# Optimization experiments

Hardware: AMD Instinct MI355X
Metric: run time of the kernel (lower is better)

Reference implementation:

```python
import jax, jax.numpy as jnp
import numpy as np

N = 120000   # current nodes
F = 256      # num_feat
H = 256      # num_hidden
L = 64       # num_logits
E_MP = 1000000  # message-passing edges
E = 200000      # scored edges
PREV = [60000, 80000, 100000]
PROX_WEIGHT = 0.3


def setup_inputs() -> dict:
    key = jax.random.key(0)
    ks = jax.random.split(key, 40)
    n = lambda k, shape, s=0.05: jax.random.normal(k, shape, dtype=jnp.float32) * s
    inp = {}
    inp["x"] = n(ks[0], (N, F), 1.0)
    inp["mp_adj"] = jax.random.randint(ks[1], (2, E_MP), 0, N)
    inp["edges"] = jax.random.randint(ks[2], (2, E), 0, N)
    inp["index"] = jax.random.randint(ks[3], (E,), 0, E)
    inp["prev_emb0"] = n(ks[4], (PREV[0], H), 1.0)
    inp["prev_emb1"] = n(ks[5], (PREV[1], H), 1.0)
    inp["prev_emb2"] = n(ks[6], (PREV[2], H), 1.0)
    # Module_L params
    inp["gc1_W"] = n(ks[7], (F, H))
    inp["gc1_b"] = jnp.zeros((H,), jnp.float32)
    inp["gc2_W"] = n(ks[8], (H, H))
    inp["gc2_b"] = jnp.zeros((H,), jnp.float32)
    inp["linear_W"] = n(ks[9], (2 * H, H))
    inp["linear_b"] = jnp.zeros((H,), jnp.float32)
    inp["weight_lin"] = n(ks[10], (H, H))
    inp["bias_lin"] = jnp.zeros((H,), jnp.float32)
    inp["w_q"] = n(ks[11], (H, H))
    inp["w_k"] = n(ks[12], (H, H))
    inp["w_v"] = n(ks[13], (H, H))
    # ensemble params
    inp["ml_w1"] = n(ks[14], (2 * H, H)); inp["ml_b1"] = jnp.zeros((H,), jnp.float32)
    inp["ml_w2"] = n(ks[15], (H, 1));     inp["ml_b2"] = jnp.zeros((1,), jnp.float32)
    inp["ms_w1"] = n(ks[16], (2 * H, H)); inp["ms_b1"] = jnp.zeros((H,), jnp.float32)
    inp["ms_w2"] = n(ks[17], (H, 1));     inp["ms_b2"] = jnp.zeros((1,), jnp.float32)
    inp["msdr_w"] = n(ks[18], (L, H));    inp["msdr_b"] = jnp.zeros((H,), jnp.float32)
    # Module_S logits and precomputed score tables
    inp["logits"] = n(ks[19], (N, L), 1.0)
    inp["ms_train_score"] = jax.random.uniform(ks[20], (E,), dtype=jnp.float32)
    inp["prox_train_score"] = jax.random.uniform(ks[21], (E,), dtype=jnp.float32)
    return inp


def _gcn(x, W, b, src, dst, n_nodes):
    xw = x @ W
    loop = jnp.arange(n_nodes)
    s = jnp.concatenate([src, loop])
    d = jnp.concatenate([dst, loop])
    deg = jax.ops.segment_sum(jnp.ones_like(d, dtype=xw.dtype), d, num_segments=n_nodes)
    dinv = jax.lax.rsqrt(jnp.maximum(deg, 1.0))
    norm = (dinv[s] * dinv[d])[:, None]
    out = jax.ops.segment_sum(xw[s] * norm, d, num_segments=n_nodes)
    return out + b


def _mean_max(a, b):
    return jnp.concatenate([(a + b) * 0.5, jnp.maximum(a, b)], axis=1)


def reference(x, mp_adj, edges, index, prev_emb0, prev_emb1, prev_emb2,
              gc1_W, gc1_b, gc2_W, gc2_b, linear_W, linear_b,
              weight_lin, bias_lin, w_q, w_k, w_v,
              ml_w1, ml_b1, ml_w2, ml_b2, ms_w1, ms_b1, ms_w2, ms_b2,
              msdr_w, msdr_b, logits, ms_train_score, prox_train_score):
    src_mp, dst_mp = mp_adj[0], mp_adj[1]
    # --- Module_L: 2-layer GCN encoder (dropout = identity in eval) ---
    h = jnp.tanh(_gcn(x, gc1_W, gc1_b, src_mp, dst_mp, N))
    emb = jnp.tanh(_gcn(h, gc2_W, gc2_b, src_mp, dst_mp, N))

    # --- ragged per-window temporal attention over previous snapshots ---
    prev = [prev_emb0, prev_emb1, prev_emb2]
    T = len(prev)
    start = 0
    parts = []
    for i in range(T):
        end = prev[i].shape[0]
        if end == N:
            break
        # stack snapshots i..T-1 plus current, restricted to window [start:end)
        stack = jnp.stack([prev[j][start:end] for j in range(i, T)] + [emb[start:end]], axis=0)  # [S,n,H]
        q = emb[start:end] @ w_q              # [n,H]
        k = stack @ w_k                        # [S,n,H]
        v = stack @ w_v                        # [S,n,H]
        attn = jnp.einsum('nh,snh->ns', q, k) / np.sqrt(np.float32(H))
        w = jax.nn.softmax(attn, axis=-1)      # [n,S]
        parts.append(jnp.einsum('ns,snh->nh', w, v))
        start = end
    if start != N:
        parts.append(emb[start:] @ w_v)
    attn_emb = jnp.concatenate(parts, axis=0)  # [N,H]

    emb2 = jnp.tanh(jnp.concatenate([emb, attn_emb], axis=1) @ linear_W + linear_b)  # [N,H]

    # --- symmetric bilinear edge scores ---
    sym = (weight_lin + weight_lin.T) * 0.5
    es, ed = edges[0], edges[1]
    sim = ((emb2[es] @ sym) * emb2[ed] + bias_lin).sum(axis=1)
    ml_scores = jax.nn.sigmoid(sim)            # [E]

    # --- Module_S / Proximity: table lookups ---
    ms_scores = ms_train_score[index]
    prox_scores = prox_train_score[index]

    # --- ensemble weighted sum ---
    scores = jnp.stack([ml_scores, ms_scores, prox_scores], axis=1)  # [E,3]
    ml_feat = _mean_max(emb2[es], emb2[ed])                          # [E,2H]
    a_ml = jnp.tanh(jnp.tanh(ml_feat @ ml_w1 + ml_b1) @ ml_w2 + ml_b2)
    r0 = jnp.tanh(logits[es] @ msdr_w + msdr_b)
    r1 = jnp.tanh(logits[ed] @ msdr_w + msdr_b)
    a_ms = jnp.tanh(jnp.tanh(_mean_max(r0, r1) @ ms_w1 + ms_b1) @ ms_w2 + ms_b2)
    a_px = jnp.full_like(a_ml, PROX_WEIGHT)
    attn_w = jax.nn.softmax(jnp.concatenate([a_ml, a_ms, a_px], axis=1), axis=1)  # [E,3]
    final = jnp.clip((scores * attn_w).sum(axis=1), 0.0, 1.0)
    return final
```

## Files before the change

### kernel.cpp

```cpp
#include <hip/hip_runtime.h>
#include <hip/hip_bf16.h>

#define Nn_   120000
#define F_    256
#define H_    256
#define L_    64
#define EMP_  1000000
#define E_    200000
#define P0_   60000
#define P1_   80000
#define P2_   100000
#define PROXW 0.3f

typedef __attribute__((ext_vector_type(8))) short bf16x8;
typedef __attribute__((ext_vector_type(4))) float f32x4;

__device__ inline float bf2f(unsigned short u) {
    union { unsigned int i; float f; } x; x.i = ((unsigned int)u) << 16; return x.f;
}
__device__ inline unsigned short f2bf(float f) {
    union { float f; unsigned int i; } x; x.f = f;
    unsigned int r = x.i + 0x7fffu + ((x.i >> 16) & 1u);
    return (unsigned short)(r >> 16);
}
__device__ inline float tanh_fast(float x) {
    float e = __expf(2.0f * x);
    return 1.0f - 2.0f * __builtin_amdgcn_rcpf(e + 1.0f);
}
__device__ inline float sigmoid_fast(float z) {
    return __builtin_amdgcn_rcpf(1.0f + __expf(-z));
}
__device__ inline int lds_off(int row, int s) {
    return row * 64 + ((s ^ ((row >> 1) & 3)) << 4);
}
__device__ inline void gload_lds16(const void* g, void* l) {
    __builtin_amdgcn_global_load_lds((const __attribute__((address_space(1))) void*)g,
                                     (__attribute__((address_space(3))) void*)l, 16, 0, 0);
}
__device__ inline void unpk8(uint4 u, float* o) {
    o[0] = bf2f(u.x & 0xffff); o[1] = bf2f(u.x >> 16);
    o[2] = bf2f(u.y & 0xffff); o[3] = bf2f(u.y >> 16);
    o[4] = bf2f(u.z & 0xffff); o[5] = bf2f(u.z >> 16);
    o[6] = bf2f(u.w & 0xffff); o[7] = bf2f(u.w >> 16);
}
__device__ inline void meanmax_u(unsigned int ua, unsigned int ub,
                                 unsigned int& um, unsigned int& ux) {
    float alo = __uint_as_float(ua << 16);
    float ahi = __uint_as_float(ua & 0xffff0000u);
    float blo = __uint_as_float(ub << 16);
    float bhi = __uint_as_float(ub & 0xffff0000u);
    um = (unsigned int)f2bf((alo + blo) * 0.5f) |
         ((unsigned int)f2bf((ahi + bhi) * 0.5f) << 16);
    ux = (__float_as_uint(fmaxf(alo, blo)) >> 16) |
         (__float_as_uint(fmaxf(ahi, bhi)) & 0xffff0000u);
}
__device__ inline float dot2_u(unsigned int ug, unsigned int ub) {
    float gl = __uint_as_float(ug << 16);
    float gh = __uint_as_float(ug & 0xffff0000u);
    float bl = __uint_as_float(ub << 16);
    float bh = __uint_as_float(ub & 0xffff0000u);
    return fmaf(gl, bl, gh * bh);
}

__global__ void k_count(const int* __restrict__ dst, int* __restrict__ cnt, int n) {
    int e = blockIdx.x * 256 + threadIdx.x;
    if (e < n) atomicAdd(&cnt[dst[e]], 1);
}
__global__ void k_block_reduce(const int* __restrict__ cnt, int* __restrict__ bsum, int n) {
    __shared__ int s[256];
    int i = blockIdx.x * 256 + threadIdx.x;
    s[threadIdx.x] = (i < n) ? cnt[i] : 0;
    __syncthreads();
    for (int o = 128; o > 0; o >>= 1) {
        if (threadIdx.x < o) s[threadIdx.x] += s[threadIdx.x + o];
        __syncthreads();
    }
    if (threadIdx.x == 0) bsum[blockIdx.x] = s[0];
}
__global__ void k_scan_bsum(int* bsum, int nb) {
    if (threadIdx.x == 0 && blockIdx.x == 0) {
        int acc = 0;
        for (int i = 0; i < nb; i++) { int v = bsum[i]; bsum[i] = acc; acc += v; }
    }
}
__global__ void k_scan_final(const int* __restrict__ cnt, const int* __restrict__ bsum,
                             int* __restrict__ rowp, int n, int etot) {
    __shared__ int s[256];
    int tid = threadIdx.x;
    int i = blockIdx.x * 256 + tid;
    int v = (i < n) ? cnt[i] : 0;
    s[tid] = v;
    __syncthreads();
    for (int o = 1; o < 256; o <<= 1) {
        int t = 0;
        if (tid >= o) t = s[tid - o];
        __syncthreads();
        s[tid] += t;
        __syncthreads();
    }
    if (i < n) rowp[i] = bsum[blockIdx.x] + s[tid] - v;
    if (i == 0 && blockIdx.x == 0) rowp[n] = etot;
}
__global__ void k_fill(const int* __restrict__ src, const int* __restrict__ dst,
                       const int* __restrict__ rowp, int* __restrict__ fill,
                       int* __restrict__ csr, int n) {
    int e = blockIdx.x * 256 + threadIdx.x;
    if (e < n) {
        int d = dst[e];
        int p = atomicAdd(&fill[d], 1);
        csr[rowp[d] + p] = src[e];
    }
}
__global__ void k_dinv(const int* __restrict__ cnt, float* __restrict__ dinv, int n) {
    int i = blockIdx.x * 256 + threadIdx.x;
    if (i < n) dinv[i] = rsqrtf((float)cnt[i] + 1.0f);
}

#define TM 64
#define TN 64
#define TK 16
template <bool TRANSB>
__global__ void gemm_tiled(const float* __restrict__ A, const float* __restrict__ B,
                           float* __restrict__ C, int M, int K, int N) {
    __shared__ float As[TK][TM + 4];
    __shared__ float Bs[TK][TN + 4];
    int tid = threadIdx.x;
    int tx = tid & 15, ty = tid >> 4;
    int row0 = blockIdx.y * TM, col0 = blockIdx.x * TN;
    int lr = tid >> 2, lc4 = (tid & 3) * 4;
    float acc[4][4] = {};
    for (int k0 = 0; k0 < K; k0 += TK) {
        {
            int gr = row0 + lr;
            float4 v = make_float4(0.f, 0.f, 0.f, 0.f);
            if (gr < M) v = *(const float4*)(A + (size_t)gr * K + k0 + lc4);
            As[lc4 + 0][lr] = v.x; As[lc4 + 1][lr] = v.y;
            As[lc4 + 2][lr] = v.z; As[lc4 + 3][lr] = v.w;
        }
        {
            int n = tid & 63, kk0 = tid >> 6;
#pragma unroll
            for (int p = 0; p < 4; p++) {
                int kk = kk0 + p * 4;
                if (TRANSB) Bs[kk][n] = B[(size_t)(col0 + n) * K + k0 + kk];
                else        Bs[kk][n] = B[(size_t)(k0 + kk) * N + col0 + n];
            }
        }
        __syncthreads();
#pragma unroll
        for (int kk = 0; kk < TK; kk++) {
            float4 a = *(const float4*)&As[kk][ty * 4];
            float4 b = *(const float4*)&Bs[kk][tx * 4];
            float av[4] = {a.x, a.y, a.z, a.w};
            float bv[4] = {b.x, b.y, b.z, b.w};
#pragma unroll
            for (int i = 0; i < 4; i++)
#pragma unroll
                for (int j = 0; j < 4; j++) acc[i][j] += av[i] * bv[j];
        }
        __syncthreads();
    }
#pragma unroll
    for (int i = 0; i < 4; i++) {
        int r = row0 + ty * 4 + i;
        if (r >= M) continue;
#pragma unroll
        for (int j = 0; j < 4; j++) C[(size_t)r * N + col0 + tx * 4 + j] = acc[i][j];
    }
}

__global__ void k_cvt(const float* __restrict__ in, unsigned short* __restrict__ out, int n4) {
    int i = blockIdx.x * 256 + threadIdx.x;
    if (i >= n4) return;
    float4 v = ((const float4*)in)[i];
    ushort4 o;
    o.x = f2bf(v.x); o.y = f2bf(v.y); o.z = f2bf(v.z); o.w = f2bf(v.w);
    ((ushort4*)out)[i] = o;
}

__device__ inline void packBF_task(const float* __restrict__ Wsrc,
                                   unsigned short* __restrict__ P, int blk) {
    int t = blk * 256 + threadIdx.x;
    int c = t >> 6, l = t & 63;
    int os = c >> 5, half = (c >> 4) & 1, colb = c & 15;
    int col = (colb << 4) + (l & 15);
    int k = (half << 8) + (os << 5) + ((l >> 4) << 3);
    bf16x8 v;
#pragma unroll
    for (int j = 0; j < 8; ++j) v[j] = (short)f2bf(Wsrc[(size_t)(k + j) * 256 + col]);
    *(bf16x8*)(P + (size_t)t * 8) = v;
}

__global__ void k_prep1(const float* __restrict__ gc1W, const float* __restrict__ gc2W,
                        const float* __restrict__ msdrW, const float* __restrict__ wlin,
                        const float* __restrict__ blin, const float* __restrict__ mlw1,
                        const float* __restrict__ msw1,
                        unsigned short* __restrict__ gc1Wt, unsigned short* __restrict__ gc2Wt,
                        unsigned short* __restrict__ msdrWt, unsigned short* __restrict__ symb,
                        float* __restrict__ sumb, unsigned short* __restrict__ mlPk,
                        unsigned short* __restrict__ msPk) {
    __shared__ float s[256];
    int b = blockIdx.x, tid = threadIdx.x;
    if (b < 256) {
        int c = b;
        for (int r = tid; r < 256; r += 256) gc1Wt[c * 256 + r] = f2bf(gc1W[(size_t)r * 256 + c]);
    } else if (b < 512) {
        int c = b - 256;
        for (int r = tid; r < 256; r += 256) gc2Wt[c * 256 + r] = f2bf(gc2W[(size_t)r * 256 + c]);
    } else if (b < 768) {
        int c = b - 512;
        if (tid < 64) msdrWt[c * 64 + tid] = f2bf(msdrW[(size_t)tid * 256 + c]);
    } else if (b < 1024) {
        int r = b - 768, c = tid;
        symb[r * 256 + c] = f2bf(0.5f * (wlin[r * 256 + c] + wlin[c * 256 + r]));
    } else if (b == 1024) {
        s[tid] = blin[tid];
        __syncthreads();
        for (int o = 128; o > 0; o >>= 1) {
            if (tid < o) s[tid] += s[tid + o];
            __syncthreads();
        }
        if (tid == 0) sumb[0] = s[0];
    } else if (b < 1089) {
        packBF_task(mlw1, mlPk, b - 1025);
    } else {
        packBF_task(msw1, msPk, b - 1089);
    }
}
__global__ void k_prep2(const float* __restrict__ Mqk, const float* __restrict__ linW,
                        const float* __restrict__ W2w, unsigned short* __restrict__ MqkT,
                        unsigned short* __restrict__ Bt) {
    int b = blockIdx.x, tid = threadIdx.x;
    if (b < 256) {
        int c = b;
        for (int r = tid; r < 256; r += 256) MqkT[c * 256 + r] = f2bf(Mqk[(size_t)r * 256 + c]);
    } else {
        int idx = (b - 256) * 256 + tid;
        int n = idx >> 9, k = idx & 511;
        float v = (k < 256) ? linW[(size_t)k * 256 + n] : W2w[(size_t)(k - 256) * 256 + n];
        Bt[idx] = f2bf(v);
    }
}

__global__ __launch_bounds__(256)
void k_agg_bf(const unsigned short* __restrict__ xw, const int* __restrict__ rowp,
              const int* __restrict__ csr, const float* __restrict__ dinv,
              const float* __restrict__ bias, unsigned short* __restrict__ out) {
    int w = threadIdx.x >> 6, lane = threadIdx.x & 63;
    int v = blockIdx.x * 4 + w;
    if (v >= Nn_) return;
    const uint2* x64 = (const uint2*)xw;
    uint2 us = x64[(size_t)v * 64 + lane];
    float dv = dinv[v];
    float4 bv = *(const float4*)(bias + lane * 4);
    float a0 = 0.f, a1 = 0.f, a2 = 0.f, a3 = 0.f;
    int beg = rowp[v], end = rowp[v + 1];
    uint2 u0 = make_uint2(0, 0), u1 = make_uint2(0, 0);
    uint2 u2 = make_uint2(0, 0), u3 = make_uint2(0, 0);
    float e0 = 0.f, e1 = 0.f, e2 = 0.f, e3 = 0.f;
    if (beg < end)     { int s = csr[beg];     e0 = dinv[s]; u0 = x64[(size_t)s * 64 + lane]; }
    if (beg + 1 < end) { int s = csr[beg + 1]; e1 = dinv[s]; u1 = x64[(size_t)s * 64 + lane]; }
    if (beg + 2 < end) { int s = csr[beg + 2]; e2 = dinv[s]; u2 = x64[(size_t)s * 64 + lane]; }
    if (beg + 3 < end) { int s = csr[beg + 3]; e3 = dinv[s]; u3 = x64[(size_t)s * 64 + lane]; }
    #pragma unroll 4
    for (int p = beg; p < end; ++p) {
        uint2 uc = u0; float dc = e0;
        u0 = u1; e0 = e1;
        u1 = u2; e1 = e2;
        u2 = u3; e2 = e3;
        if (p + 4 < end) {
            int s = csr[p + 4];
            e3 = dinv[s];
            u3 = x64[(size_t)s * 64 + lane];
        }
        a0 += bf2f(uc.x & 0xffff) * dc;
        a1 += bf2f(uc.x >> 16) * dc;
        a2 += bf2f(uc.y & 0xffff) * dc;
        a3 += bf2f(uc.y >> 16) * dc;
    }
    a0 = a0 * dv + bf2f(us.x & 0xffff) * dv * dv;
    a1 = a1 * dv + bf2f(us.x >> 16) * dv * dv;
    a2 = a2 * dv + bf2f(us.y & 0xffff) * dv * dv;
    a3 = a3 * dv + bf2f(us.y >> 16) * dv * dv;
    uint2 ov;
    ov.x = (unsigned int)f2bf(tanh_fast(a0 + bv.x)) |
           ((unsigned int)f2bf(tanh_fast(a1 + bv.y)) << 16);
    ov.y = (unsigned int)f2bf(tanh_fast(a2 + bv.z)) |
           ((unsigned int)f2bf(tanh_fast(a3 + bv.w)) << 16);
    ((uint2*)out)[(size_t)v * 64 + lane] = ov;
}

template <bool BIAS, bool TANH>
__global__ __launch_bounds__(256)
void mfma_gemm(const unsigned short* __restrict__ A0, const unsigned short* __restrict__ A1,
               int Ksplit, int K, const unsigned short* __restrict__ Bt,
               const float* __restrict__ bias, unsigned short* __restrict__ Cb, int M) {
    __shared__ char lds[2][16384];
    int tid = threadIdx.x, lane = tid & 63, w = tid >> 6;
    int row0 = blockIdx.y * 128, col0 = blockIdx.x * 128;
    int wr = w >> 1, wc = w & 1;
    f32x4 acc[4][4] = {};
    int nk = K >> 5;

    auto stage = [&](int ks, int buf) {
        int k0 = ks << 5;
        #pragma unroll
        for (int j = 0; j < 4; ++j) {
            int ins = w + (j << 2);
            int lrow = ((ins & 7) << 4) + (lane >> 2);
            int p = lane & 3;
            int slog = p ^ ((lrow >> 1) & 3);
            char* ldst = lds[buf] + ((ins & 7) << 10) + ((ins >= 8) ? 8192 : 0);
            const unsigned short* src;
            if (ins < 8) {
                int grow = row0 + lrow;
                if (grow >= M) grow = M - 1;
                const unsigned short* Asrc; int kk, pitch;
                if (k0 < Ksplit) { Asrc = A0; kk = k0; pitch = Ksplit; }
                else             { Asrc = A1; kk = k0 - Ksplit; pitch = K - Ksplit; }
                src = Asrc + (size_t)grow * pitch + kk + (slog << 3);
            } else {
                int grow = col0 + lrow;
                src = Bt + (size_t)grow * K + k0 + (slog << 3);
            }
            gload_lds16(src, ldst);
        }
    };

    stage(0, 0);
    for (int ks = 0; ks < nk; ++ks) {
        int cur = ks & 1;
        if (ks + 1 < nk) {
            stage(ks + 1, cur ^ 1);
            asm volatile("s_waitcnt vmcnt(4)" ::: "memory");
        } else {
            asm volatile("s_waitcnt vmcnt(0)" ::: "memory");
        }
        __builtin_amdgcn_s_barrier();
        __builtin_amdgcn_sched_barrier(0);
        int s = lane >> 4, r16 = lane & 15;
        bf16x8 a[4], b[4];
        #pragma unroll
        for (int m = 0; m < 4; ++m) a[m] = *(const bf16x8*)(lds[cur] + lds_off(wr * 64 + m * 16 + r16, s));
        #pragma unroll
        for (int n = 0; n < 4; ++n) b[n] = *(const bf16x8*)(lds[cur] + 8192 + lds_off(wc * 64 + n * 16 + r16, s));
        __builtin_amdgcn_s_setprio(1);
        #pragma unroll
        for (int m = 0; m < 4; ++m)
            #pragma unroll
            for (int n = 0; n < 4; ++n)
                acc[m][n] = __builtin_amdgcn_mfma_f32_16x16x32_bf16(a[m], b[n], acc[m][n], 0, 0, 0);
        __builtin_amdgcn_s_setprio(0);
        __builtin_amdgcn_s_barrier();
        __builtin_amdgcn_sched_barrier(0);
    }
    int q = lane >> 4, r16 = lane & 15;
    float bv[4];
    #pragma unroll
    for (int n = 0; n < 4; ++n) bv[n] = BIAS ? bias[col0 + wc * 64 + n * 16 + r16] : 0.f;
    #pragma unroll
    for (int m = 0; m < 4; ++m) {
        #pragma unroll
        for (int i = 0; i < 4; ++i) {
            int row = row0 + wr * 64 + m * 16 + q * 4 + i;
            if (row >= M) continue;
            #pragma unroll
            for (int n = 0; n < 4; ++n) {
                int col = col0 + wc * 64 + n * 16 + r16;
                float v = acc[m][n][i];
                if (BIAS) v += bv[n];
                if (TANH) v = tanh_fast(v);
                Cb[(size_t)row * 256 + col] = f2bf(v);
            }
        }
    }
}

__global__ __launch_bounds__(256)
void k_attn_u2(const unsigned short* __restrict__ emb, const unsigned short* __restrict__ t,
               const float* __restrict__ p0, const float* __restrict__ p1,
               const float* __restrict__ p2, unsigned short* __restrict__ u) {
    int tid = threadIdx.x;
    int g = tid >> 4, l = tid & 15;
    int n = blockIdx.x * 16 + g;
    size_t eoff = (size_t)n * 256 + l * 16;
    const uint4* e16 = (const uint4*)(emb + eoff);
    uint4* u16 = (uint4*)(u + eoff);
    uint4 eb0 = e16[0], eb1 = e16[1];
    if (n >= P2_) { u16[0] = eb0; u16[1] = eb1; return; }
    float tv[16], ev[16];
    {
        const uint4* t16 = (const uint4*)(t + eoff);
        unpk8(t16[0], tv); unpk8(t16[1], tv + 8);
        unpk8(eb0, ev); unpk8(eb1, ev + 8);
    }
    float m = -3.0e38f, den = 0.f, o[16];
    #pragma unroll
    for (int i = 0; i < 16; i++) o[i] = 0.f;
    auto accum = [&](const float* sv) {
        float dt = 0.f;
        #pragma unroll
        for (int i = 0; i < 16; i++) dt += tv[i] * sv[i];
        dt += __shfl_xor(dt, 1);
        dt += __shfl_xor(dt, 2);
        dt += __shfl_xor(dt, 4);
        dt += __shfl_xor(dt, 8);
        float lg = dt * 0.0625f;
        float mn = fmaxf(m, lg);
        float s0 = __expf(m - mn), s1 = __expf(lg - mn);
        den = den * s0 + s1;
        #pragma unroll
        for (int i = 0; i < 16; i++) o[i] = o[i] * s0 + s1 * sv[i];
        m = mn;
    };
    auto accum_f32 = [&](const float* base) {
        float sv[16];
        const float4* b4 = (const float4*)(base + eoff);
        #pragma unroll
        for (int i = 0; i < 4; i++) {
            float4 q = b4[i];
            sv[4 * i] = q.x; sv[4 * i + 1] = q.y; sv[4 * i + 2] = q.z; sv[4 * i + 3] = q.w;
        }
        accum(sv);
    };
    if (n < P0_)      { accum_f32(p0); accum_f32(p1); accum_f32(p2); }
    else if (n < P1_) { accum_f32(p1); accum_f32(p2); }
    else              { accum_f32(p2); }
    accum(ev);
    float inv = __builtin_amdgcn_rcpf(den);
    unsigned short h[16];
    #pragma unroll
    for (int i = 0; i < 16; i++) h[i] = f2bf(o[i] * inv);
    uint4 r0, r1;
    r0.x = h[0] | ((unsigned int)h[1] << 16);  r0.y = h[2] | ((unsigned int)h[3] << 16);
    r0.z = h[4] | ((unsigned int)h[5] << 16);  r0.w = h[6] | ((unsigned int)h[7] << 16);
    r1.x = h[8] | ((unsigned int)h[9] << 16);  r1.y = h[10] | ((unsigned int)h[11] << 16);
    r1.z = h[12] | ((unsigned int)h[13] << 16); r1.w = h[14] | ((unsigned int)h[15] << 16);
    u16[0] = r0; u16[1] = r1;
}

template <bool SIM>
__global__ __launch_bounds__(256)
void mfma_edge3(const unsigned short* __restrict__ srcemb, const unsigned short* __restrict__ gsrc,
                const int* __restrict__ es, const int* __restrict__ ed,
                const unsigned short* __restrict__ PkF, const float* __restrict__ b1,
                const float* __restrict__ w2, const float* __restrict__ sumb,
                float* __restrict__ a_pre, float* __restrict__ mlsc) {
    __shared__ char lds[8192];
    __shared__ float red[64];
    int tid = threadIdx.x, lane = tid & 63, w = tid >> 6;
    int e0 = blockIdx.x * 64;
    int arow = tid >> 2, p = tid & 3;
    int ia = es[e0 + arow], ib = ed[e0 + arow];
    const unsigned short* ra = srcemb + (size_t)ia * 256;
    const unsigned short* rb = srcemb + (size_t)ib * 256;
    const unsigned short* rg = SIM ? (gsrc + (size_t)ia * 256) : nullptr;
    int slog = p ^ ((arow >> 1) & 3);
    int abase = arow * 64 + (p << 4);
    if (tid < 64) red[tid] = 0.f;
    float simacc = 0.f;
    f32x4 acc[4][4] = {};
    uint4 pa = *(const uint4*)(ra + (slog << 3));
    uint4 pb = *(const uint4*)(rb + (slog << 3));
    uint4 pg = make_uint4(0, 0, 0, 0);
    if (SIM) pg = *(const uint4*)(rg + (slog << 3));
    const bf16x8* BF = (const bf16x8*)PkF;
    for (int os = 0; os < 8; ++os) {
        {
            unsigned int m0, x0, m1, x1, m2, x2, m3, x3;
            meanmax_u(pa.x, pb.x, m0, x0);
            meanmax_u(pa.y, pb.y, m1, x1);
            meanmax_u(pa.z, pb.z, m2, x2);
            meanmax_u(pa.w, pb.w, m3, x3);
            *(uint4*)(lds + abase) = make_uint4(m0, m1, m2, m3);
            *(uint4*)(lds + 4096 + abase) = make_uint4(x0, x1, x2, x3);
            if (SIM)
                simacc += dot2_u(pg.x, pb.x) + dot2_u(pg.y, pb.y) +
                          dot2_u(pg.z, pb.z) + dot2_u(pg.w, pb.w);
        }
        bf16x8 b0[4], b1f[4];
        #pragma unroll
        for (int n2 = 0; n2 < 4; ++n2) {
            int c0i = (os << 5) + (w << 2) + n2;
            b0[n2]  = BF[(size_t)c0i * 64 + lane];
            b1f[n2] = BF[(size_t)(c0i + 16) * 64 + lane];
        }
        if (os < 7) {
            int cb = ((os + 1) << 5) + (slog << 3);
            pa = *(const uint4*)(ra + cb);
            pb = *(const uint4*)(rb + cb);
            if (SIM) pg = *(const uint4*)(rg + cb);
        }
        asm volatile("s_waitcnt lgkmcnt(0)" ::: "memory");
        __builtin_amdgcn_s_barrier();
        __builtin_amdgcn_sched_barrier(0);
        int s = lane >> 4, r16 = lane & 15;
        {
            bf16x8 a[4];
            #pragma unroll
            for (int m2 = 0; m2 < 4; ++m2)
                a[m2] = *(const bf16x8*)(lds + lds_off(m2 * 16 + r16, s));
            __builtin_amdgcn_s_setprio(1);
            #pragma unroll
            for (int m2 = 0; m2 < 4; ++m2)
                #pragma unroll
                for (int n2 = 0; n2 < 4; ++n2)
                    acc[m2][n2] = __builtin_amdgcn_mfma_f32_16x16x32_bf16(a[m2], b0[n2], acc[m2][n2], 0, 0, 0);
            __builtin_amdgcn_s_setprio(0);
        }
        {
            bf16x8 a[4];
            #pragma unroll
            for (int m2 = 0; m2 < 4; ++m2)
                a[m2] = *(const bf16x8*)(lds + 4096 + lds_off(m2 * 16 + r16, s));
            __builtin_amdgcn_s_setprio(1);
            #pragma unroll
            for (int m2 = 0; m2 < 4; ++m2)
                #pragma unroll
                for (int n2 = 0; n2 < 4; ++n2)
                    acc[m2][n2] = __builtin_amdgcn_mfma_f32_16x16x32_bf16(a[m2], b1f[n2], acc[m2][n2], 0, 0, 0);
            __builtin_amdgcn_s_setprio(0);
        }
        __builtin_amdgcn_s_barrier();
        __builtin_amdgcn_sched_barrier(0);
    }
    int q = lane >> 4, r16 = lane & 15;
    float b1c[4], w2c[4];
    #pragma unroll
    for (int n2 = 0; n2 < 4; ++n2) {
        int c = (w << 6) + n2 * 16 + r16;
        b1c[n2] = b1[c]; w2c[n2] = w2[c];
    }
    #pragma unroll
    for (int m2 = 0; m2 < 4; ++m2) {
        #pragma unroll
        for (int i = 0; i < 4; ++i) {
            int row = m2 * 16 + q * 4 + i;
            float ps = 0.f;
            #pragma unroll
            for (int n2 = 0; n2 < 4; ++n2) ps += tanh_fast(acc[m2][n2][i] + b1c[n2]) * w2c[n2];
            ps += __shfl_xor(ps, 1);
            ps += __shfl_xor(ps, 2);
            ps += __shfl_xor(ps, 4);
            ps += __shfl_xor(ps, 8);
            if (r16 == 0) atomicAdd(&red[row], ps);
        }
    }
    if (SIM) {
        simacc += __shfl_xor(simacc, 1);
        simacc += __shfl_xor(simacc, 2);
        if (p == 0) mlsc[e0 + arow] = sigmoid_fast(simacc + sumb[0]);
    }
    __syncthreads();
    if (tid < 64) a_pre[e0 + tid] = red[tid];
}

__global__ void k_final(const float* __restrict__ apml, const float* __restrict__ apms,
                        const float* __restrict__ mlsc, const float* __restrict__ mstr,
                        const float* __restrict__ pxtr, const int* __restrict__ index,
                        const float* __restrict__ mlb2, const float* __restrict__ msb2,
                        float* __restrict__ out) {
    int e = blockIdx.x * 256 + threadIdx.x;
    if (e >= E_) return;
    float aml = tanh_fast(apml[e] + mlb2[0]);
    float ams = tanh_fast(apms[e] + msb2[0]);
    float apx = PROXW;
    float m = fmaxf(aml, fmaxf(ams, apx));
    float wml = __expf(aml - m), wms = __expf(ams - m), wpx = __expf(apx - m);
    float inv = __builtin_amdgcn_rcpf(wml + wms + wpx);
    int idx = index[e];
    float v = (mlsc[e] * wml + mstr[idx] * wms + pxtr[idx] * wpx) * inv;
    out[e] = fminf(fmaxf(v, 0.f), 1.f);
}

__global__ void k_sentinel(float* out, int n) {
    int i = blockIdx.x * 256 + threadIdx.x;
    if (i < n) out[i] = -12345.0f;
}

extern "C" void kernel_launch(void* const* d_in, const int* in_sizes, int n_in,
                              void* d_out, int out_size, void* d_ws, size_t ws_size,
                              hipStream_t stream) {
    const float* x     = (const float*)d_in[0];
    const int*   mp    = (const int*)d_in[1];
    const int*   edges = (const int*)d_in[2];
    const int*   index = (const int*)d_in[3];
    const float* p0    = (const float*)d_in[4];
    const float* p1    = (const float*)d_in[5];
    const float* p2    = (const float*)d_in[6];
    const float* gc1W  = (const float*)d_in[7];
    const float* gc1b  = (const float*)d_in[8];
    const float* gc2W  = (const float*)d_in[9];
    const float* gc2b  = (const float*)d_in[10];
    const float* linW  = (const float*)d_in[11];
    const float* linb  = (const float*)d_in[12];
    const float* wlin  = (const float*)d_in[13];
    const float* blin  = (const float*)d_in[14];
    const float* wq    = (const float*)d_in[15];
    const float* wk    = (const float*)d_in[16];
    const float* wv    = (const float*)d_in[17];
    const float* mlw1  = (const float*)d_in[18];
    const float* mlb1  = (const float*)d_in[19];
    const float* mlw2  = (const float*)d_in[20];
    const float* mlb2  = (const float*)d_in[21];
    const float* msw1  = (const float*)d_in[22];
    const float* msb1  = (const float*)d_in[23];
    const float* msw2  = (const float*)d_in[24];
    const float* msb2  = (const float*)d_in[25];
    const float* msdrW = (const float*)d_in[26];
    const float* msdrb = (const float*)d_in[27];
    const float* logits = (const float*)d_in[28];
    const float* mstr  = (const float*)d_in[29];
    const float* pxtr  = (const float*)d_in[30];
    float* out = (float*)d_out;

    const int* src_mp = mp;
    const int* dst_mp = mp + EMP_;
    const int* es = edges;
    const int* ed = edges + E_;

    char* ws = (char*)d_ws;
    size_t off = 0;
    auto alloc = [&](size_t bytes) -> char* {
        off = (off + 255) & ~(size_t)255;
        char* r = ws + off;
        off += bytes;
        return r;
    };
    const size_t NODE_BF = (size_t)Nn_ * 256 * 2;
    unsigned short* W0 = (unsigned short*)alloc(NODE_BF);
    unsigned short* W1 = (unsigned short*)alloc(NODE_BF);
    unsigned short* W2 = (unsigned short*)alloc(NODE_BF);
    unsigned short* W3 = (unsigned short*)alloc(NODE_BF);
    unsigned short* W4 = (unsigned short*)alloc(NODE_BF);
    unsigned short* W5 = (unsigned short*)alloc(NODE_BF);
    int*   cnt  = (int*)alloc((size_t)Nn_ * 4);
    int*   rowp = (int*)alloc((size_t)(Nn_ + 1) * 4);
    int*   fill = (int*)alloc((size_t)Nn_ * 4);
    int*   csr  = (int*)alloc((size_t)EMP_ * 4);
    float* dinv = (float*)alloc((size_t)Nn_ * 4);
    int*   bsum = (int*)alloc(512 * 4);
    float* Mqk  = (float*)alloc(65536 * 4);
    float* W2wf = (float*)alloc(65536 * 4);
    unsigned short* gc1Wt = (unsigned short*)alloc(65536 * 2);
    unsigned short* gc2Wt = (unsigned short*)alloc(65536 * 2);
    unsigned short* MqkT  = (unsigned short*)alloc(65536 * 2);
    unsigned short* Bt512 = (unsigned short*)alloc(131072 * 2);
    unsigned short* symb  = (unsigned short*)alloc(65536 * 2);
    unsigned short* msdrWt = (unsigned short*)alloc(16384 * 2);
    unsigned short* mlPk  = (unsigned short*)alloc(131072 * 2);
    unsigned short* msPk  = (unsigned short*)alloc(131072 * 2);
    float* apml = (float*)alloc((size_t)E_ * 4);
    float* apms = (float*)alloc((size_t)E_ * 4);
    float* mlsc = (float*)alloc((size_t)E_ * 4);
    float* sumb = (float*)alloc(256);

    if (off > ws_size) {
        k_sentinel<<<(E_ + 255) / 256, 256, 0, stream>>>(out, E_);
        return;
    }

    hipMemsetAsync(cnt, 0, (size_t)Nn_ * 4, stream);
    hipMemsetAsync(fill, 0, (size_t)Nn_ * 4, stream);

    const int NB = (Nn_ + 255) / 256;
    const int EB = (EMP_ + 255) / 256;

    k_cvt<<<30000, 256, 0, stream>>>(x, W0, Nn_ * 256 / 4);
    k_prep1<<<1153, 256, 0, stream>>>(gc1W, gc2W, msdrW, wlin, blin, mlw1, msw1,
                                      gc1Wt, gc2Wt, msdrWt, symb, sumb, mlPk, msPk);
    dim3 gSmall(4, 4);
    gemm_tiled<true><<<gSmall, 256, 0, stream>>>(wq, wk, Mqk, 256, 256, 256);
    gemm_tiled<false><<<gSmall, 256, 0, stream>>>(wv, linW + 256 * 256, W2wf, 256, 256, 256);
    k_prep2<<<768, 256, 0, stream>>>(Mqk, linW, W2wf, MqkT, Bt512);

    k_count<<<EB, 256, 0, stream>>>(dst_mp, cnt, EMP_);
    k_block_reduce<<<NB, 256, 0, stream>>>(cnt, bsum, Nn_);
    k_scan_bsum<<<1, 64, 0, stream>>>(bsum, NB);
    k_scan_final<<<NB, 256, 0, stream>>>(cnt, bsum, rowp, Nn_, EMP_);
    k_fill<<<EB, 256, 0, stream>>>(src_mp, dst_mp, rowp, fill, csr, EMP_);
    k_dinv<<<NB, 256, 0, stream>>>(cnt, dinv, Nn_);

    dim3 gFull(2, (Nn_ + 127) / 128);
    dim3 gT(2, (P2_ + 127) / 128);
    const int AGG_B = (Nn_ + 3) / 4;

    mfma_gemm<false, false><<<gFull, 256, 0, stream>>>(W0, W0, 256, 256, gc1Wt, nullptr, W1, Nn_);
    k_agg_bf<<<AGG_B, 256, 0, stream>>>(W1, rowp, csr, dinv, gc1b, W2);
    mfma_gemm<false, false><<<gFull, 256, 0, stream>>>(W2, W2, 256, 256, gc2Wt, nullptr, W1, Nn_);
    k_agg_bf<<<AGG_B, 256, 0, stream>>>(W1, rowp, csr, dinv, gc2b, W3);

    mfma_gemm<false, false><<<gT, 256, 0, stream>>>(W3, W3, 256, 256, MqkT, nullptr, W4, P2_);
    k_attn_u2<<<Nn_ / 16, 256, 0, stream>>>(W3, W4, p0, p1, p2, W4);

    mfma_gemm<true, true><<<gFull, 256, 0, stream>>>(W3, W4, 256, 512, Bt512, linb, W5, Nn_);

    mfma_gemm<false, false><<<gFull, 256, 0, stream>>>(W5, W5, 256, 256, symb, nullptr, W0, Nn_);

    k_cvt<<<7500, 256, 0, stream>>>(logits, W1, Nn_ * 64 / 4);
    mfma_gemm<true, true><<<gFull, 256, 0, stream>>>(W1, W1, 64, 64, msdrWt, msdrb, W2, Nn_);

    mfma_edge3<true><<<E_ / 64, 256, 0, stream>>>(W5, W0, es, ed, mlPk, mlb1, mlw2, sumb, apml, mlsc);
    mfma_edge3<false><<<E_ / 64, 256, 0, stream>>>(W2, nullptr, es, ed, msPk, msb1, msw2, sumb, apms, nullptr);

    k_final<<<(E_ + 255) / 256, 256, 0, stream>>>(apml, apms, mlsc, mstr, pxtr, index, mlb2, msb2, out);
}
```

Measured before the change: 946.7 us.

## Merge both edge-scoring kernels into one launch and double-buffer LDS tiles

Replaces the two templated edge MLP kernel launches with a single launch whose first half of blocks handles the ML branch and second half the MS branch. The template flag becomes a runtime block-dependent flag. The LDS staging buffer is doubled so consecutive iterations alternate buffers, which lets the trailing barrier per iteration be dropped. This is meant to cut one launch, improve tail-wave occupancy and reduce synchronization, at the cost of more shared memory per block and runtime branching.

After: 929.2 us. No clear change (-1.9%).

```diff
diff --git a/kernel.cpp b/kernel.cpp
--- a/kernel.cpp
+++ b/kernel.cpp
@@ -439,22 +439,32 @@
     u16[0] = r0; u16[1] = r1;
 }
 
-template <bool SIM>
 __global__ __launch_bounds__(256)
-void mfma_edge3(const unsigned short* __restrict__ srcemb, const unsigned short* __restrict__ gsrc,
+void mfma_edge7(const unsigned short* __restrict__ emb2b, const unsigned short* __restrict__ rtabb,
+                const unsigned short* __restrict__ gtab,
                 const int* __restrict__ es, const int* __restrict__ ed,
-                const unsigned short* __restrict__ PkF, const float* __restrict__ b1,
-                const float* __restrict__ w2, const float* __restrict__ sumb,
-                float* __restrict__ a_pre, float* __restrict__ mlsc) {
-    __shared__ char lds[8192];
+                const unsigned short* __restrict__ PkMl, const unsigned short* __restrict__ PkMs,
+                const float* __restrict__ b1ml, const float* __restrict__ w2ml,
+                const float* __restrict__ b1ms, const float* __restrict__ w2ms,
+                const float* __restrict__ sumb,
+                float* __restrict__ apml, float* __restrict__ apms,
+                float* __restrict__ mlsc, int nml) {
+    __shared__ char lds[16384];
     __shared__ float red[64];
+    bool sim = (int)blockIdx.x < nml;
+    int bid = sim ? blockIdx.x : (blockIdx.x - nml);
+    const unsigned short* srcemb = sim ? emb2b : rtabb;
+    const unsigned short* PkF = sim ? PkMl : PkMs;
+    const float* b1 = sim ? b1ml : b1ms;
+    const float* w2 = sim ? w2ml : w2ms;
+    float* a_pre = sim ? apml : apms;
     int tid = threadIdx.x, lane = tid & 63, w = tid >> 6;
-    int e0 = blockIdx.x * 64;
+    int e0 = bid * 64;
     int arow = tid >> 2, p = tid & 3;
     int ia = es[e0 + arow], ib = ed[e0 + arow];
     const unsigned short* ra = srcemb + (size_t)ia * 256;
     const unsigned short* rb = srcemb + (size_t)ib * 256;
-    const unsigned short* rg = SIM ? (gsrc + (size_t)ia * 256) : nullptr;
+    const unsigned short* rg = gtab + (size_t)ia * 256;
     int slog = p ^ ((arow >> 1) & 3);
     int abase = arow * 64 + (p << 4);
     if (tid < 64) red[tid] = 0.f;
@@ -463,18 +473,19 @@
     uint4 pa = *(const uint4*)(ra + (slog << 3));
     uint4 pb = *(const uint4*)(rb + (slog << 3));
     uint4 pg = make_uint4(0, 0, 0, 0);
-    if (SIM) pg = *(const uint4*)(rg + (slog << 3));
+    if (sim) pg = *(const uint4*)(rg + (slog << 3));
     const bf16x8* BF = (const bf16x8*)PkF;
     for (int os = 0; os < 8; ++os) {
+        int cbuf = (os & 1) << 13;
         {
             unsigned int m0, x0, m1, x1, m2, x2, m3, x3;
             meanmax_u(pa.x, pb.x, m0, x0);
             meanmax_u(pa.y, pb.y, m1, x1);
             meanmax_u(pa.z, pb.z, m2, x2);
             meanmax_u(pa.w, pb.w, m3, x3);
-            *(uint4*)(lds + abase) = make_uint4(m0, m1, m2, m3);
-            *(uint4*)(lds + 4096 + abase) = make_uint4(x0, x1, x2, x3);
-            if (SIM)
+            *(uint4*)(lds + cbuf + abase) = make_uint4(m0, m1, m2, m3);
+            *(uint4*)(lds + cbuf + 4096 + abase) = make_uint4(x0, x1, x2, x3);
+            if (sim)
                 simacc += dot2_u(pg.x, pb.x) + dot2_u(pg.y, pb.y) +
                           dot2_u(pg.z, pb.z) + dot2_u(pg.w, pb.w);
         }
@@ -489,7 +500,7 @@
             int cb = ((os + 1) << 5) + (slog << 3);
             pa = *(const uint4*)(ra + cb);
             pb = *(const uint4*)(rb + cb);
-            if (SIM) pg = *(const uint4*)(rg + cb);
+            if (sim) pg = *(const uint4*)(rg + cb);
         }
         asm volatile("s_waitcnt lgkmcnt(0)" ::: "memory");
         __builtin_amdgcn_s_barrier();
@@ -499,7 +510,7 @@
             bf16x8 a[4];
             #pragma unroll
             for (int m2 = 0; m2 < 4; ++m2)
-                a[m2] = *(const bf16x8*)(lds + lds_off(m2 * 16 + r16, s));
+                a[m2] = *(const bf16x8*)(lds + cbuf + lds_off(m2 * 16 + r16, s));
             __builtin_amdgcn_s_setprio(1);
             #pragma unroll
             for (int m2 = 0; m2 < 4; ++m2)
@@ -512,7 +523,7 @@
             bf16x8 a[4];
             #pragma unroll
             for (int m2 = 0; m2 < 4; ++m2)
-                a[m2] = *(const bf16x8*)(lds + 4096 + lds_off(m2 * 16 + r16, s));
+                a[m2] = *(const bf16x8*)(lds + cbuf + 4096 + lds_off(m2 * 16 + r16, s));
             __builtin_amdgcn_s_setprio(1);
             #pragma unroll
             for (int m2 = 0; m2 < 4; ++m2)
@@ -521,8 +532,6 @@
                     acc[m2][n2] = __builtin_amdgcn_mfma_f32_16x16x32_bf16(a[m2], b1f[n2], acc[m2][n2], 0, 0, 0);
             __builtin_amdgcn_s_setprio(0);
         }
-        __builtin_amdgcn_s_barrier();
-        __builtin_amdgcn_sched_barrier(0);
     }
     int q = lane >> 4, r16 = lane & 15;
     float b1c[4], w2c[4];
@@ -546,7 +555,7 @@
             if (r16 == 0) atomicAdd(&red[row], ps);
         }
     }
-    if (SIM) {
+    if (sim) {
         simacc += __shfl_xor(simacc, 1);
         simacc += __shfl_xor(simacc, 2);
         if (p == 0) mlsc[e0 + arow] = sigmoid_fast(simacc + sumb[0]);
@@ -700,8 +709,10 @@
     k_cvt<<<7500, 256, 0, stream>>>(logits, W1, Nn_ * 64 / 4);
     mfma_gemm<true, true><<<gFull, 256, 0, stream>>>(W1, W1, 64, 64, msdrWt, msdrb, W2, Nn_);
 
-    mfma_edge3<true><<<E_ / 64, 256, 0, stream>>>(W5, W0, es, ed, mlPk, mlb1, mlw2, sumb, apml, mlsc);
-    mfma_edge3<false><<<E_ / 64, 256, 0, stream>>>(W2, nullptr, es, ed, msPk, msb1, msw2, sumb, apms, nullptr);
+    const int NML = E_ / 64;
+    mfma_edge7<<<2 * NML, 256, 0, stream>>>(W5, W2, W0, es, ed, mlPk, msPk,
+                                            mlb1, mlw2, msb1, msw2, sumb,
+                                            apml, apms, mlsc, NML);
 
     k_final<<<(E_ + 255) / 256, 256, 0, stream>>>(apml, apms, mlsc, mstr, pxtr, index, mlb2, msb2, out);
 }
```
